# Kernel optimization log

Measured on AMD Instinct MI355X. Metric: run time of the kernel, lower is better.

The kernel has to match this reference:

```python
import jax, jax.numpy as jnp
import numpy as np

# Levelized timing graph: L levels of P pins, each pin at level l>0 has K fanin
# arcs from level l-1. src_idx holds level-local source pin indices.
L = 32          # logic depth
P = 131072      # pins per level  (n_pins = L*P = 4,194,304)
K = 2           # fanin arcs per pin
N_NETS = 1000000
TIMING_PERIOD = jnp.float32(10.0)
NEG = jnp.float32(-1e30)
POS = jnp.float32(1e30)


def setup_inputs() -> dict:
    key = jax.random.key(0)
    k1, k2, k3, k4 = jax.random.split(key, 4)
    # per-pin arc delays (ns-scale)
    pin_delays = jax.random.uniform(k1, (L * P,), dtype=jnp.float32) * 0.5
    # fanin sources: level-local indices into the previous level
    src_idx = jax.random.randint(k2, (L - 1, P, K), 0, P, dtype=jnp.int32)
    # net id of each timing arc
    net_ids = jax.random.randint(k3, (L - 1, P, K), 0, N_NETS, dtype=jnp.int32)
    net_mask_ignore_large = jax.random.uniform(k4, (N_NETS,)) < 0.01
    return {
        "pin_delays": pin_delays,
        "src_idx": src_idx,
        "net_ids": net_ids,
        "net_mask_ignore_large": net_mask_ignore_large,
    }


def reference(pin_delays, src_idx, net_ids, net_mask_ignore_large):
    delays = pin_delays.reshape(L, P)              # [L, P]
    valid = ~net_mask_ignore_large[net_ids]        # [L-1, P, K] arcs on ignored nets are skipped

    # ---- forward (arrival) propagation: max over fanin ----
    arr = [delays[0]]                              # source pins launch at their own delay
    for l in range(1, L):
        contrib = arr[-1][src_idx[l - 1]] + delays[l][:, None]   # [P, K]
        contrib = jnp.where(valid[l - 1], contrib, NEG)
        arr.append(jnp.maximum(jnp.max(contrib, axis=-1), delays[l]))
    arrival = jnp.stack(arr)                       # [L, P]

    # ---- backward (required) propagation: min over fanout (scatter-min) ----
    req = [None] * L
    req[L - 1] = jnp.full((P,), TIMING_PERIOD, dtype=jnp.float32)  # endpoints
    for l in range(L - 2, -1, -1):
        contrib = req[l + 1] - delays[l + 1]                        # [P]
        c = jnp.where(valid[l], contrib[:, None], POS)              # [P, K]
        r = jnp.full((P,), TIMING_PERIOD, dtype=jnp.float32)
        r = r.at[src_idx[l].ravel()].min(c.ravel())
        req[l] = r
    required = jnp.stack(req)                      # [L, P]

    pin_arrivals = arrival.reshape(-1)
    pin_requires = required.reshape(-1)
    pin_slacks = pin_requires - pin_arrivals
    return pin_arrivals, pin_requires, pin_slacks, net_mask_ignore_large
```

## Files before the change

kernel.cpp:

```cpp
#include <hip/hip_runtime.h>

constexpr int L = 32;
constexpr int P = 131072;
constexpr int LP = L * P;
constexpr int NNETS = 1000000;
constexpr float TPER = 10.0f;
constexpr float NEGV = -1e30f;

__device__ __forceinline__ void atomic_min_f32(float* addr, float val) {
  if (val >= 0.0f) {
    atomicMin(reinterpret_cast<int*>(addr), __float_as_int(val));
  } else {
    atomicMax(reinterpret_cast<unsigned int*>(addr), __float_as_uint(val));
  }
}

__global__ __launch_bounds__(256) void sta_init(
    const float* __restrict__ delays, const int* __restrict__ mask,
    float* __restrict__ out) {
  int i4 = (blockIdx.x * blockDim.x + threadIdx.x) * 4;
  if (i4 < LP) {
    float4 ten = {TPER, TPER, TPER, TPER};
    *reinterpret_cast<float4*>(out + LP + i4) = ten;
    if (i4 < P) {
      *reinterpret_cast<float4*>(out + i4) =
          *reinterpret_cast<const float4*>(delays + i4);
    }
  }
  if (i4 < NNETS) {
    int4 m = *reinterpret_cast<const int4*>(mask + i4);
    float4 f = {(float)(m.x != 0), (float)(m.y != 0), (float)(m.z != 0),
                (float)(m.w != 0)};
    *reinterpret_cast<float4*>(out + 3 * LP + i4) = f;
  }
}

__global__ __launch_bounds__(256) void sta_step(
    const float* __restrict__ delays, const int* __restrict__ src,
    const int* __restrict__ net, const int* __restrict__ mask,
    float* __restrict__ out, int i) {
  const int p = blockIdx.x * blockDim.x + threadIdx.x;
  float* arr = out;
  float* req = out + LP;
  const int lf = i;
  const int lb = L - 1 - i;

  {
    const float d = delays[lf * P + p];
    const int2 s = *reinterpret_cast<const int2*>(src + (size_t)(lf - 1) * P * 2 + p * 2);
    const int2 n = *reinterpret_cast<const int2*>(net + (size_t)(lf - 1) * P * 2 + p * 2);
    const float* ap = arr + (lf - 1) * P;
    const float v0 = mask[n.x] ? NEGV : ap[s.x] + d;
    const float v1 = mask[n.y] ? NEGV : ap[s.y] + d;
    arr[lf * P + p] = fmaxf(fmaxf(v0, v1), d);
  }

  {
    const float d = delays[(lb + 1) * P + p];
    const float r = req[(lb + 1) * P + p];
    const float c = r - d;
    const int2 s = *reinterpret_cast<const int2*>(src + (size_t)lb * P * 2 + p * 2);
    const int2 n = *reinterpret_cast<const int2*>(net + (size_t)lb * P * 2 + p * 2);
    float* rp = req + lb * P;
    if (!mask[n.x]) atomic_min_f32(rp + s.x, c);
    if (!mask[n.y]) atomic_min_f32(rp + s.y, c);
  }
}

__global__ __launch_bounds__(256) void sta_slack(float* __restrict__ out) {
  int i4 = (blockIdx.x * blockDim.x + threadIdx.x) * 4;
  if (i4 < LP) {
    float4 a = *reinterpret_cast<const float4*>(out + i4);
    float4 r = *reinterpret_cast<const float4*>(out + LP + i4);
    float4 s = {r.x - a.x, r.y - a.y, r.z - a.z, r.w - a.w};
    *reinterpret_cast<float4*>(out + 2 * LP + i4) = s;
  }
}

extern "C" void kernel_launch(void* const* d_in, const int* in_sizes, int n_in,
                              void* d_out, int out_size, void* d_ws, size_t ws_size,
                              hipStream_t stream) {
  const float* delays = (const float*)d_in[0];
  const int* src = (const int*)d_in[1];
  const int* net = (const int*)d_in[2];
  const int* mask = (const int*)d_in[3];
  float* out = (float*)d_out;

  sta_init<<<LP / 1024, 256, 0, stream>>>(delays, mask, out);
  for (int i = 1; i < L; ++i) {
    sta_step<<<P / 256, 256, 0, stream>>>(delays, src, net, mask, out, i);
  }
  sta_slack<<<LP / 1024, 256, 0, stream>>>(out);
}
```

Before: 615.9 us.

## Precompute masked source indices in a pre-pass and split forward/backward threads

Result: faster. 593.7 us (-3.6%).

```diff
diff --git a/kernel.cpp b/kernel.cpp
--- a/kernel.cpp
+++ b/kernel.cpp
@@ -3,15 +3,32 @@
 constexpr int L = 32;
 constexpr int P = 131072;
 constexpr int LP = L * P;
+constexpr int NARC = (L - 1) * P * 2;
 constexpr int NNETS = 1000000;
 constexpr float TPER = 10.0f;
 constexpr float NEGV = -1e30f;
+constexpr int SRCMASK = P - 1;
 
 __device__ __forceinline__ void atomic_min_f32(float* addr, float val) {
   if (val >= 0.0f) {
     atomicMin(reinterpret_cast<int*>(addr), __float_as_int(val));
   } else {
     atomicMax(reinterpret_cast<unsigned int*>(addr), __float_as_uint(val));
+  }
+}
+
+__global__ __launch_bounds__(256) void sta_pre(
+    const int* __restrict__ src, const int* __restrict__ net,
+    const int* __restrict__ mask, int* __restrict__ esrc) {
+  int a4 = (blockIdx.x * blockDim.x + threadIdx.x) * 4;
+  if (a4 < NARC) {
+    int4 s = *reinterpret_cast<const int4*>(src + a4);
+    int4 n = *reinterpret_cast<const int4*>(net + a4);
+    s.x |= mask[n.x] ? 0x80000000 : 0;
+    s.y |= mask[n.y] ? 0x80000000 : 0;
+    s.z |= mask[n.z] ? 0x80000000 : 0;
+    s.w |= mask[n.w] ? 0x80000000 : 0;
+    *reinterpret_cast<int4*>(esrc + a4) = s;
   }
 }
 
@@ -36,6 +53,34 @@
 }
 
 __global__ __launch_bounds__(256) void sta_step(
+    const float* __restrict__ delays, const int* __restrict__ esrc,
+    float* __restrict__ out, int i) {
+  const int t = blockIdx.x * blockDim.x + threadIdx.x;
+  float* arr = out;
+  float* req = out + LP;
+  const int lf = i;
+  const int lb = L - 1 - i;
+  if (t < P) {
+    const int p = t;
+    const float d = delays[lf * P + p];
+    const int2 s = *reinterpret_cast<const int2*>(esrc + (size_t)(lf - 1) * P * 2 + p * 2);
+    const float* ap = arr + (lf - 1) * P;
+    float v0 = ap[s.x & SRCMASK] + d;
+    float v1 = ap[s.y & SRCMASK] + d;
+    v0 = (s.x < 0) ? NEGV : v0;
+    v1 = (s.y < 0) ? NEGV : v1;
+    arr[lf * P + p] = fmaxf(fmaxf(v0, v1), d);
+  } else {
+    const int p = t - P;
+    const float c = req[(lb + 1) * P + p] - delays[(lb + 1) * P + p];
+    const int2 s = *reinterpret_cast<const int2*>(esrc + (size_t)lb * P * 2 + p * 2);
+    float* rp = req + lb * P;
+    if (s.x >= 0) atomic_min_f32(rp + s.x, c);
+    if (s.y >= 0) atomic_min_f32(rp + s.y, c);
+  }
+}
+
+__global__ __launch_bounds__(256) void sta_step_direct(
     const float* __restrict__ delays, const int* __restrict__ src,
     const int* __restrict__ net, const int* __restrict__ mask,
     float* __restrict__ out, int i) {
@@ -44,7 +89,6 @@
   float* req = out + LP;
   const int lf = i;
   const int lb = L - 1 - i;
-
   {
     const float d = delays[lf * P + p];
     const int2 s = *reinterpret_cast<const int2*>(src + (size_t)(lf - 1) * P * 2 + p * 2);
@@ -54,11 +98,8 @@
     const float v1 = mask[n.y] ? NEGV : ap[s.y] + d;
     arr[lf * P + p] = fmaxf(fmaxf(v0, v1), d);
   }
-
   {
-    const float d = delays[(lb + 1) * P + p];
-    const float r = req[(lb + 1) * P + p];
-    const float c = r - d;
+    const float c = req[(lb + 1) * P + p] - delays[(lb + 1) * P + p];
     const int2 s = *reinterpret_cast<const int2*>(src + (size_t)lb * P * 2 + p * 2);
     const int2 n = *reinterpret_cast<const int2*>(net + (size_t)lb * P * 2 + p * 2);
     float* rp = req + lb * P;
@@ -85,10 +126,20 @@
   const int* net = (const int*)d_in[2];
   const int* mask = (const int*)d_in[3];
   float* out = (float*)d_out;
+  int* esrc = (int*)d_ws;
+
+  const bool use_esrc = ws_size >= (size_t)NARC * sizeof(int);
 
   sta_init<<<LP / 1024, 256, 0, stream>>>(delays, mask, out);
-  for (int i = 1; i < L; ++i) {
-    sta_step<<<P / 256, 256, 0, stream>>>(delays, src, net, mask, out, i);
+  if (use_esrc) {
+    sta_pre<<<NARC / 4 / 256, 256, 0, stream>>>(src, net, mask, esrc);
+    for (int i = 1; i < L; ++i) {
+      sta_step<<<2 * P / 256, 256, 0, stream>>>(delays, esrc, out, i);
+    }
+  } else {
+    for (int i = 1; i < L; ++i) {
+      sta_step_direct<<<P / 256, 256, 0, stream>>>(delays, src, net, mask, out, i);
+    }
   }
   sta_slack<<<LP / 1024, 256, 0, stream>>>(out);
 }
```

## Fuse STA propagation into one cooperative persistent kernel with grid barriers

Applied to the files above, without the earlier changes.

Result: slower. 721.5 us (+17.1%).

```diff
diff --git a/kernel.cpp b/kernel.cpp
--- a/kernel.cpp
+++ b/kernel.cpp
@@ -4,14 +4,114 @@
 constexpr int P = 131072;
 constexpr int LP = L * P;
 constexpr int NNETS = 1000000;
+constexpr int NBITW = NNETS / 32;
+constexpr int NBLK = 512;
+constexpr int TPB = 256;
 constexpr float TPER = 10.0f;
 constexpr float NEGV = -1e30f;
+constexpr int WS_CNT = 32768;
+constexpr int WS_FLAG = WS_CNT + 32;
+
+__device__ __forceinline__ float agent_load_f(const float* p) {
+  return __hip_atomic_load(p, __ATOMIC_RELAXED, __HIP_MEMORY_SCOPE_AGENT);
+}
+__device__ __forceinline__ void agent_store_f(float* p, float v) {
+  __hip_atomic_store(p, v, __ATOMIC_RELAXED, __HIP_MEMORY_SCOPE_AGENT);
+}
+__device__ __forceinline__ void agent_store_i(int* p, int v) {
+  __hip_atomic_store(p, v, __ATOMIC_RELAXED, __HIP_MEMORY_SCOPE_AGENT);
+}
 
 __device__ __forceinline__ void atomic_min_f32(float* addr, float val) {
   if (val >= 0.0f) {
     atomicMin(reinterpret_cast<int*>(addr), __float_as_int(val));
   } else {
     atomicMax(reinterpret_cast<unsigned int*>(addr), __float_as_uint(val));
+  }
+}
+
+__device__ __forceinline__ void gbar(int* cnt, int* flag, int epoch) {
+  asm volatile("s_waitcnt vmcnt(0)" ::: "memory");
+  __syncthreads();
+  if (threadIdx.x == 0) {
+    int old = __hip_atomic_fetch_add(cnt, 1, __ATOMIC_RELAXED,
+                                     __HIP_MEMORY_SCOPE_AGENT);
+    if (old == epoch * NBLK - 1) {
+      __hip_atomic_store(flag, epoch, __ATOMIC_RELAXED,
+                         __HIP_MEMORY_SCOPE_AGENT);
+    } else {
+      while (__hip_atomic_load(flag, __ATOMIC_RELAXED,
+                               __HIP_MEMORY_SCOPE_AGENT) < epoch) {
+        __builtin_amdgcn_s_sleep(2);
+      }
+    }
+  }
+  __syncthreads();
+}
+
+__global__ __launch_bounds__(TPB) void sta_persist(
+    const float* __restrict__ delays, const int* __restrict__ src,
+    const int* __restrict__ net, const int* __restrict__ mask,
+    float* __restrict__ out, int* __restrict__ ws) {
+  const int p = blockIdx.x * TPB + threadIdx.x;
+  float* arr = out;
+  float* req = out + LP;
+  float* slk = out + 2 * LP;
+  float* mf = out + 3 * LP;
+  int* bits = ws;
+  int* cnt = ws + WS_CNT;
+  int* flag = ws + WS_FLAG;
+
+  if (p < NBITW) {
+    const int* mp = mask + p * 32;
+    unsigned w = 0;
+#pragma unroll
+    for (int j = 0; j < 32; ++j) w |= (mp[j] ? 1u : 0u) << j;
+    agent_store_i(bits + p, (int)w);
+  }
+  agent_store_f(arr + p, delays[p]);
+#pragma unroll
+  for (int l = 0; l < L; ++l) agent_store_f(req + l * P + p, TPER);
+  {
+    const int base = p * 8;
+#pragma unroll
+    for (int j = 0; j < 8; ++j) {
+      const int idx = base + j;
+      if (idx < NNETS) mf[idx] = mask[idx] ? 1.0f : 0.0f;
+    }
+  }
+  gbar(cnt, flag, 1);
+
+  for (int i = 1; i < L; ++i) {
+    const int lf = i, lb = L - 1 - i;
+    {
+      const float d = delays[lf * P + p];
+      const int2 s = *reinterpret_cast<const int2*>(src + (size_t)(lf - 1) * P * 2 + p * 2);
+      const int2 n = *reinterpret_cast<const int2*>(net + (size_t)(lf - 1) * P * 2 + p * 2);
+      const float* ap = arr + (size_t)(lf - 1) * P;
+      float v0 = ap[s.x] + d;
+      float v1 = ap[s.y] + d;
+      if ((bits[n.x >> 5] >> (n.x & 31)) & 1) v0 = NEGV;
+      if ((bits[n.y >> 5] >> (n.y & 31)) & 1) v1 = NEGV;
+      agent_store_f(arr + (size_t)lf * P + p, fmaxf(fmaxf(v0, v1), d));
+    }
+    {
+      const float rq = agent_load_f(req + (size_t)(lb + 1) * P + p);
+      const float d = delays[(lb + 1) * P + p];
+      const float c = rq - d;
+      const int2 s = *reinterpret_cast<const int2*>(src + (size_t)lb * P * 2 + p * 2);
+      const int2 n = *reinterpret_cast<const int2*>(net + (size_t)lb * P * 2 + p * 2);
+      float* rp = req + (size_t)lb * P;
+      if (!((bits[n.x >> 5] >> (n.x & 31)) & 1)) atomic_min_f32(rp + s.x, c);
+      if (!((bits[n.y >> 5] >> (n.y & 31)) & 1)) atomic_min_f32(rp + s.y, c);
+    }
+    gbar(cnt, flag, i + 1);
+  }
+
+  for (int l = 0; l < L; ++l) {
+    const float a = arr[(size_t)l * P + p];
+    const float r = agent_load_f(req + (size_t)l * P + p);
+    slk[(size_t)l * P + p] = r - a;
   }
 }
 
@@ -22,10 +122,9 @@
   if (i4 < LP) {
     float4 ten = {TPER, TPER, TPER, TPER};
     *reinterpret_cast<float4*>(out + LP + i4) = ten;
-    if (i4 < P) {
+    if (i4 < P)
       *reinterpret_cast<float4*>(out + i4) =
           *reinterpret_cast<const float4*>(delays + i4);
-    }
   }
   if (i4 < NNETS) {
     int4 m = *reinterpret_cast<const int4*>(mask + i4);
@@ -35,16 +134,14 @@
   }
 }
 
-__global__ __launch_bounds__(256) void sta_step(
+__global__ __launch_bounds__(256) void sta_step_direct(
     const float* __restrict__ delays, const int* __restrict__ src,
     const int* __restrict__ net, const int* __restrict__ mask,
     float* __restrict__ out, int i) {
   const int p = blockIdx.x * blockDim.x + threadIdx.x;
   float* arr = out;
   float* req = out + LP;
-  const int lf = i;
-  const int lb = L - 1 - i;
-
+  const int lf = i, lb = L - 1 - i;
   {
     const float d = delays[lf * P + p];
     const int2 s = *reinterpret_cast<const int2*>(src + (size_t)(lf - 1) * P * 2 + p * 2);
@@ -54,11 +151,8 @@
     const float v1 = mask[n.y] ? NEGV : ap[s.y] + d;
     arr[lf * P + p] = fmaxf(fmaxf(v0, v1), d);
   }
-
   {
-    const float d = delays[(lb + 1) * P + p];
-    const float r = req[(lb + 1) * P + p];
-    const float c = r - d;
+    const float c = req[(lb + 1) * P + p] - delays[(lb + 1) * P + p];
     const int2 s = *reinterpret_cast<const int2*>(src + (size_t)lb * P * 2 + p * 2);
     const int2 n = *reinterpret_cast<const int2*>(net + (size_t)lb * P * 2 + p * 2);
     float* rp = req + lb * P;
@@ -85,10 +179,20 @@
   const int* net = (const int*)d_in[2];
   const int* mask = (const int*)d_in[3];
   float* out = (float*)d_out;
+  int* ws = (int*)d_ws;
 
+  if (ws_size >= (size_t)(WS_FLAG + 32) * sizeof(int)) {
+    hipMemsetAsync((char*)d_ws + (size_t)WS_CNT * sizeof(int), 0, 256, stream);
+    void* args[] = {(void*)&delays, (void*)&src, (void*)&net,
+                    (void*)&mask, (void*)&out, (void*)&ws};
+    hipError_t e = hipLaunchCooperativeKernel((const void*)sta_persist,
+                                              dim3(NBLK), dim3(TPB), args, 0,
+                                              stream);
+    if (e == hipSuccess) return;
+    (void)hipGetLastError();
+  }
   sta_init<<<LP / 1024, 256, 0, stream>>>(delays, mask, out);
-  for (int i = 1; i < L; ++i) {
-    sta_step<<<P / 256, 256, 0, stream>>>(delays, src, net, mask, out, i);
-  }
+  for (int i = 1; i < L; ++i)
+    sta_step_direct<<<P / 256, 256, 0, stream>>>(delays, src, net, mask, out, i);
   sta_slack<<<LP / 1024, 256, 0, stream>>>(out);
 }
```

## Replace scatter-min backward pass with CSR fanout gather and bit-packed mask

Applied to the files above, without the earlier changes.

New measurement: 1.436 ms. 133% more time.

```diff
diff --git a/kernel.cpp b/kernel.cpp
--- a/kernel.cpp
+++ b/kernel.cpp
@@ -3,9 +3,23 @@
 constexpr int L = 32;
 constexpr int P = 131072;
 constexpr int LP = L * P;
+constexpr int LM1 = L - 1;
+constexpr int APL = 2 * P;
+constexpr int NARC = LM1 * APL;
 constexpr int NNETS = 1000000;
 constexpr float TPER = 10.0f;
 constexpr float NEGV = -1e30f;
+constexpr int SRCMASK = P - 1;
+
+constexpr size_t WS_ESRC = 0;
+constexpr size_t WS_ENT  = WS_ESRC + (size_t)NARC;
+constexpr size_t WS_OFF  = WS_ENT + (size_t)LM1 * APL;
+constexpr size_t WS_CNT  = WS_OFF + (size_t)LM1 * P;
+constexpr size_t WS_CUR  = WS_CNT + (size_t)LM1 * P;
+constexpr size_t WS_RC   = WS_CUR + (size_t)LM1 * P;
+constexpr size_t WS_BITS = WS_RC + (size_t)LP;
+constexpr size_t WS_PART = WS_BITS + 32768;
+constexpr size_t WS_END  = WS_PART + (size_t)LM1 * 128;
 
 __device__ __forceinline__ void atomic_min_f32(float* addr, float val) {
   if (val >= 0.0f) {
@@ -15,17 +29,207 @@
   }
 }
 
+
 __global__ __launch_bounds__(256) void sta_init(
+    const float* __restrict__ delays, const int* __restrict__ mask,
+    float* __restrict__ out, int* __restrict__ ws) {
+  const int p = blockIdx.x * blockDim.x + threadIdx.x;
+  float* rc = reinterpret_cast<float*>(ws + WS_RC);
+  out[p] = delays[p];
+  const float dl = delays[(L - 1) * P + p];
+  out[LP + (L - 1) * P + p] = TPER;
+  rc[(L - 1) * P + p] = TPER - dl;
+  float* mf = out + 3 * LP;
+  const int base = p * 8;
+  if (base + 7 < NNETS) {
+    const int4 a = *reinterpret_cast<const int4*>(mask + base);
+    const int4 b = *reinterpret_cast<const int4*>(mask + base + 4);
+    float4 fa = {a.x ? 1.0f : 0.0f, a.y ? 1.0f : 0.0f, a.z ? 1.0f : 0.0f,
+                 a.w ? 1.0f : 0.0f};
+    float4 fb = {b.x ? 1.0f : 0.0f, b.y ? 1.0f : 0.0f, b.z ? 1.0f : 0.0f,
+                 b.w ? 1.0f : 0.0f};
+    *reinterpret_cast<float4*>(mf + base) = fa;
+    *reinterpret_cast<float4*>(mf + base + 4) = fb;
+  } else {
+    for (int j = 0; j < 8; ++j)
+      if (base + j < NNETS) mf[base + j] = mask[base + j] ? 1.0f : 0.0f;
+  }
+}
+
+__global__ __launch_bounds__(256) void sta_bits(const int* __restrict__ mask,
+                                                int* __restrict__ ws) {
+  const int t = blockIdx.x * blockDim.x + threadIdx.x;
+  const int lane = threadIdx.x & 63;
+  int* bits = ws + WS_BITS;
+#pragma unroll
+  for (int r = 0; r < 8; ++r) {
+    const int idx = r * P + t;
+    int mv = 0;
+    if (idx < NNETS) mv = mask[idx];
+    unsigned long long bal = __ballot(mv != 0);
+    if (lane == 0)
+      *reinterpret_cast<unsigned long long*>(
+          ws + WS_BITS + ((r * P + (t & ~63)) >> 5)) = bal;
+  }
+  (void)bits;
+}
+
+__global__ __launch_bounds__(256) void sta_esrc(const int* __restrict__ src,
+                                                const int* __restrict__ net,
+                                                int* __restrict__ ws) {
+  const int a4 = (blockIdx.x * blockDim.x + threadIdx.x) * 4;
+  const int* bits = ws + WS_BITS;
+  if (a4 < NARC) {
+    int4 s = *reinterpret_cast<const int4*>(src + a4);
+    int4 n = *reinterpret_cast<const int4*>(net + a4);
+    s.x |= ((bits[n.x >> 5] >> (n.x & 31)) & 1) << 31;
+    s.y |= ((bits[n.y >> 5] >> (n.y & 31)) & 1) << 31;
+    s.z |= ((bits[n.z >> 5] >> (n.z & 31)) & 1) << 31;
+    s.w |= ((bits[n.w >> 5] >> (n.w & 31)) & 1) << 31;
+    *reinterpret_cast<int4*>(ws + WS_ESRC + a4) = s;
+  }
+}
+
+__global__ __launch_bounds__(256) void sta_count(int* __restrict__ ws) {
+  const int g4 = (blockIdx.x * blockDim.x + threadIdx.x) * 4;
+  int* cnt = ws + WS_CNT;
+  if (g4 < NARC) {
+    const int4 e = *reinterpret_cast<const int4*>(ws + WS_ESRC + g4);
+#pragma unroll
+    for (int k = 0; k < 4; ++k) {
+      const int s = (&e.x)[k];
+      if (s >= 0) {
+        const int l = (g4 + k) >> 18;
+        atomicAdd(cnt + l * P + s, 1);
+      }
+    }
+  }
+}
+
+__global__ __launch_bounds__(256) void sta_scan1(int* __restrict__ ws) {
+  __shared__ int sd[256];
+  const int l = blockIdx.x >> 7;
+  const int blk = blockIdx.x & 127;
+  const int t = threadIdx.x;
+  const int base = l * P + blk * 1024;
+  const int4 c = *reinterpret_cast<const int4*>(ws + WS_CNT + base + t * 4);
+  const int s = c.x + c.y + c.z + c.w;
+  sd[t] = s;
+  __syncthreads();
+  for (int off = 1; off < 256; off <<= 1) {
+    int v = (t >= off) ? sd[t - off] : 0;
+    __syncthreads();
+    sd[t] += v;
+    __syncthreads();
+  }
+  const int ex = sd[t] - s;
+  int4 o;
+  o.x = ex;
+  o.y = ex + c.x;
+  o.z = o.y + c.y;
+  o.w = o.z + c.z;
+  *reinterpret_cast<int4*>(ws + WS_OFF + base + t * 4) = o;
+  if (t == 255) ws[WS_PART + l * 128 + blk] = sd[255];
+}
+
+__global__ __launch_bounds__(128) void sta_scan2(int* __restrict__ ws) {
+  __shared__ int sd[128];
+  const int l = blockIdx.x;
+  const int t = threadIdx.x;
+  const int v = ws[WS_PART + l * 128 + t];
+  sd[t] = v;
+  __syncthreads();
+  for (int off = 1; off < 128; off <<= 1) {
+    int u = (t >= off) ? sd[t - off] : 0;
+    __syncthreads();
+    sd[t] += u;
+    __syncthreads();
+  }
+  ws[WS_PART + l * 128 + t] = sd[t] - v;
+}
+
+__global__ __launch_bounds__(256) void sta_scan3(int* __restrict__ ws) {
+  const int l = blockIdx.x >> 7;
+  const int blk = blockIdx.x & 127;
+  const int t = threadIdx.x;
+  const int base = l * P + blk * 1024;
+  const int add = ws[WS_PART + l * 128 + blk];
+  int4 o = *reinterpret_cast<const int4*>(ws + WS_OFF + base + t * 4);
+  o.x += add; o.y += add; o.z += add; o.w += add;
+  *reinterpret_cast<int4*>(ws + WS_OFF + base + t * 4) = o;
+  *reinterpret_cast<int4*>(ws + WS_CUR + base + t * 4) = o;
+}
+
+__global__ __launch_bounds__(256) void sta_fill(int* __restrict__ ws) {
+  const int g4 = (blockIdx.x * blockDim.x + threadIdx.x) * 4;
+  int* cur = ws + WS_CUR;
+  int* ent = ws + WS_ENT;
+  if (g4 < NARC) {
+    const int4 e = *reinterpret_cast<const int4*>(ws + WS_ESRC + g4);
+#pragma unroll
+    for (int k = 0; k < 4; ++k) {
+      const int s = (&e.x)[k];
+      if (s >= 0) {
+        const int g = g4 + k;
+        const int l = g >> 18;
+        const int slot = atomicAdd(cur + l * P + s, 1);
+        ent[(size_t)l * APL + slot] = (g & (APL - 1)) >> 1;
+      }
+    }
+  }
+}
+
+__global__ __launch_bounds__(256) void sta_step(
+    const float* __restrict__ delays, float* __restrict__ out,
+    int* __restrict__ ws, int i) {
+  const int p = blockIdx.x * blockDim.x + threadIdx.x;
+  float* arr = out;
+  float* req = out + LP;
+  float* rc = reinterpret_cast<float*>(ws + WS_RC);
+  const int lf = i, lb = L - 1 - i;
+  {
+    const float d = delays[lf * P + p];
+    const int2 s2 = *reinterpret_cast<const int2*>(ws + WS_ESRC +
+                                                   (size_t)(lf - 1) * APL + p * 2);
+    const float* ap = arr + (size_t)(lf - 1) * P;
+    float v0 = ap[s2.x & SRCMASK] + d;
+    float v1 = ap[s2.y & SRCMASK] + d;
+    if (s2.x < 0) v0 = NEGV;
+    if (s2.y < 0) v1 = NEGV;
+    arr[(size_t)lf * P + p] = fmaxf(fmaxf(v0, v1), d);
+  }
+  {
+    const int b = ws[WS_OFF + lb * P + p];
+    const int e = ws[WS_CUR + lb * P + p];
+    const int* ep = ws + WS_ENT + (size_t)lb * APL;
+    const float* rcp = rc + (size_t)(lb + 1) * P;
+    float m = TPER;
+    for (int j = b; j < e; ++j) m = fminf(m, rcp[ep[j]]);
+    req[(size_t)lb * P + p] = m;
+    rc[(size_t)lb * P + p] = m - delays[lb * P + p];
+  }
+}
+
+__global__ __launch_bounds__(256) void sta_slack(float* __restrict__ out) {
+  int i4 = (blockIdx.x * blockDim.x + threadIdx.x) * 4;
+  if (i4 < LP) {
+    float4 a = *reinterpret_cast<const float4*>(out + i4);
+    float4 r = *reinterpret_cast<const float4*>(out + LP + i4);
+    float4 s = {r.x - a.x, r.y - a.y, r.z - a.z, r.w - a.w};
+    *reinterpret_cast<float4*>(out + 2 * LP + i4) = s;
+  }
+}
+
+__global__ __launch_bounds__(256) void sta_init_fb(
     const float* __restrict__ delays, const int* __restrict__ mask,
     float* __restrict__ out) {
   int i4 = (blockIdx.x * blockDim.x + threadIdx.x) * 4;
   if (i4 < LP) {
     float4 ten = {TPER, TPER, TPER, TPER};
     *reinterpret_cast<float4*>(out + LP + i4) = ten;
-    if (i4 < P) {
+    if (i4 < P)
       *reinterpret_cast<float4*>(out + i4) =
           *reinterpret_cast<const float4*>(delays + i4);
-    }
   }
   if (i4 < NNETS) {
     int4 m = *reinterpret_cast<const int4*>(mask + i4);
@@ -35,16 +239,14 @@
   }
 }
 
-__global__ __launch_bounds__(256) void sta_step(
+__global__ __launch_bounds__(256) void sta_step_direct(
     const float* __restrict__ delays, const int* __restrict__ src,
     const int* __restrict__ net, const int* __restrict__ mask,
     float* __restrict__ out, int i) {
   const int p = blockIdx.x * blockDim.x + threadIdx.x;
   float* arr = out;
   float* req = out + LP;
-  const int lf = i;
-  const int lb = L - 1 - i;
-
+  const int lf = i, lb = L - 1 - i;
   {
     const float d = delays[lf * P + p];
     const int2 s = *reinterpret_cast<const int2*>(src + (size_t)(lf - 1) * P * 2 + p * 2);
@@ -54,26 +256,13 @@
     const float v1 = mask[n.y] ? NEGV : ap[s.y] + d;
     arr[lf * P + p] = fmaxf(fmaxf(v0, v1), d);
   }
-
-  {
-    const float d = delays[(lb + 1) * P + p];
-    const float r = req[(lb + 1) * P + p];
-    const float c = r - d;
+  {
+    const float c = req[(lb + 1) * P + p] - delays[(lb + 1) * P + p];
     const int2 s = *reinterpret_cast<const int2*>(src + (size_t)lb * P * 2 + p * 2);
     const int2 n = *reinterpret_cast<const int2*>(net + (size_t)lb * P * 2 + p * 2);
     float* rp = req + lb * P;
     if (!mask[n.x]) atomic_min_f32(rp + s.x, c);
     if (!mask[n.y]) atomic_min_f32(rp + s.y, c);
-  }
-}
-
-__global__ __launch_bounds__(256) void sta_slack(float* __restrict__ out) {
-  int i4 = (blockIdx.x * blockDim.x + threadIdx.x) * 4;
-  if (i4 < LP) {
-    float4 a = *reinterpret_cast<const float4*>(out + i4);
-    float4 r = *reinterpret_cast<const float4*>(out + LP + i4);
-    float4 s = {r.x - a.x, r.y - a.y, r.z - a.z, r.w - a.w};
-    *reinterpret_cast<float4*>(out + 2 * LP + i4) = s;
   }
 }
 
@@ -85,10 +274,26 @@
   const int* net = (const int*)d_in[2];
   const int* mask = (const int*)d_in[3];
   float* out = (float*)d_out;
-
-  sta_init<<<LP / 1024, 256, 0, stream>>>(delays, mask, out);
-  for (int i = 1; i < L; ++i) {
-    sta_step<<<P / 256, 256, 0, stream>>>(delays, src, net, mask, out, i);
-  }
+  int* ws = (int*)d_ws;
+
+  if (ws_size >= WS_END * sizeof(int)) {
+    sta_init<<<P / 256, 256, 0, stream>>>(delays, mask, out, ws);
+    sta_bits<<<P / 256, 256, 0, stream>>>(mask, ws);
+    sta_esrc<<<NARC / 4 / 256, 256, 0, stream>>>(src, net, ws);
+    hipMemsetAsync((char*)d_ws + WS_CNT * sizeof(int), 0,
+                   (size_t)LM1 * P * sizeof(int), stream);
+    sta_count<<<NARC / 4 / 256, 256, 0, stream>>>(ws);
+    sta_scan1<<<LM1 * 128, 256, 0, stream>>>(ws);
+    sta_scan2<<<LM1, 128, 0, stream>>>(ws);
+    sta_scan3<<<LM1 * 128, 256, 0, stream>>>(ws);
+    sta_fill<<<NARC / 4 / 256, 256, 0, stream>>>(ws);
+    for (int i = 1; i < L; ++i)
+      sta_step<<<P / 256, 256, 0, stream>>>(delays, out, ws, i);
+    sta_slack<<<LP / 1024, 256, 0, stream>>>(out);
+    return;
+  }
+  sta_init_fb<<<LP / 1024, 256, 0, stream>>>(delays, mask, out);
+  for (int i = 1; i < L; ++i)
+    sta_step_direct<<<P / 256, 256, 0, stream>>>(delays, src, net, mask, out, i);
   sta_slack<<<LP / 1024, 256, 0, stream>>>(out);
 }
```
